# Performance work log

Hardware: AMD Instinct MI355X
Metric: run time of the kernel (lower is better)

## Reference

```python
import jax, jax.numpy as jnp
import numpy as np

N, W, D = 2048, 64, 512
TEMP = 16.0
LN_EPS = 1e-5
NORM_EPS = 1e-12


def layernorm(x, w, b):
    mu = jnp.mean(x, axis=-1, keepdims=True)
    var = jnp.mean(jnp.square(x - mu), axis=-1, keepdims=True)
    return (x - mu) * jax.lax.rsqrt(var + LN_EPS) * w + b


def l2norm(x):
    n = jnp.linalg.norm(x, axis=-1, keepdims=True)
    return x / jnp.maximum(n, NORM_EPS)


def setup_inputs() -> dict:
    key = jax.random.key(0)
    ks = jax.random.split(key, 6)
    q = jax.random.normal(ks[0], (N, D), dtype=jnp.float32)
    cm = jax.random.normal(ks[1], (W, D), dtype=jnp.float32)
    s1 = 1.0 / np.sqrt(2 * D)
    s2 = 1.0 / np.sqrt(D)
    return {
        "query_embeddings": q,
        "class_memories": cm,
        "ln1_w": jnp.ones((2 * D,), jnp.float32),
        "ln1_b": jnp.zeros((2 * D,), jnp.float32),
        "w1": jax.random.uniform(ks[2], (2 * D, D), jnp.float32, -s1, s1),
        "b1": jax.random.uniform(ks[3], (D,), jnp.float32, -s1, s1),
        "w2": jax.random.uniform(ks[4], (D, D), jnp.float32, -s2, s2),
        "b2": jax.random.uniform(ks[5], (D,), jnp.float32, -s2, s2),
        "ln2_w": jnp.ones((D,), jnp.float32),
        "ln2_b": jnp.zeros((D,), jnp.float32),
    }


def reference(query_embeddings, class_memories, ln1_w, ln1_b, w1, b1, w2, b2, ln2_w, ln2_b):
    n, w = query_embeddings.shape[0], class_memories.shape[0]
    q_exp = jnp.broadcast_to(query_embeddings[:, None, :], (n, w, D))   # [N,W,D]
    c_exp = jnp.broadcast_to(class_memories[None, :, :], (n, w, D))     # [N,W,D]
    x = jnp.concatenate([q_exp, c_exp], axis=-1)                        # [N,W,2D]
    h = layernorm(x, ln1_w, ln1_b)
    h = h @ w1 + b1                                                     # [N,W,D]
    h = jax.nn.gelu(h, approximate=False)
    h = h @ w2 + b2                                                     # [N,W,D]
    fused = layernorm(h + q_exp, ln2_w, ln2_b)
    sims = jnp.einsum('nwd,wd->nw', l2norm(fused), l2norm(class_memories))
    return TEMP * sims
```

## Files before the change

kernel.cpp:

```cpp
#include <hip/hip_runtime.h>
#include <cstdint>
#include <cstddef>


#define NQ 2048
#define NWC 64
#define DD 512
#define NCHUNK 19

typedef __attribute__((ext_vector_type(8))) short short8;
typedef __attribute__((ext_vector_type(8))) unsigned short ushort8;
typedef __attribute__((ext_vector_type(4))) float f32x4;

__device__ __forceinline__ unsigned short f2bf(float f) {
  unsigned u = __float_as_uint(f);
  u += 0x7fffu + ((u >> 16) & 1u);
  return (unsigned short)(u >> 16);
}

__device__ __forceinline__ unsigned cvtpk2(float lo, float hi) {
  unsigned r;
  asm("v_cvt_pk_bf16_f32 %0, %1, %2" : "=v"(r) : "v"(lo), "v"(hi));
  return r;
}

__device__ __forceinline__ float bf2f(unsigned short u) {
  return __uint_as_float(((unsigned)u) << 16);
}

__device__ __forceinline__ float gelu_f(float h) {
  float h2 = h * h;
  float z2 = h * fmaf(h2, 0.10295890518f, 2.30221607f);
  float e = exp2f(z2);
  return h * (e * __builtin_amdgcn_rcpf(e + 1.0f));
}

__device__ __forceinline__ float wred(float v) {
#pragma unroll
  for (int m = 1; m < 64; m <<= 1) v += __shfl_xor(v, m, 64);
  return v;
}

__device__ __forceinline__ float sel4(f32x4 v, int r) {
  float x = (r & 1) ? v[1] : v[0];
  float y = (r & 1) ? v[3] : v[2];
  return (r & 2) ? y : x;
}

__global__ __launch_bounds__(256) void k_prep(
    const float* __restrict__ q, const float* __restrict__ cm,
    const float* __restrict__ g1, const float* __restrict__ be1,
    const float* __restrict__ w1, const float* __restrict__ w2,
    const float* __restrict__ g2, const float* __restrict__ be2,
    const float* __restrict__ b2,
    float* __restrict__ Sq, float* __restrict__ SSq, float* __restrict__ qst,
    float* __restrict__ Sc, float* __restrict__ SSc, float* __restrict__ cmhg,
    float* __restrict__ c1, float* __restrict__ c2, float* __restrict__ c3,
    float* __restrict__ Gp, float* __restrict__ Cp, float* __restrict__ V,
    float* __restrict__ gg, float* __restrict__ scal) {
  const int b = blockIdx.x, tid = threadIdx.x;
  const int wv = tid >> 6, l = tid & 63;
  __shared__ float shr[3][4];
  __shared__ float s_inv;

  if (b < 256) {
    f32x4 b20 = *(const f32x4*)(b2 + l * 8);
    f32x4 b21 = *(const f32x4*)(b2 + l * 8 + 4);
    f32x4 g20 = *(const f32x4*)(g2 + l * 8);
    f32x4 g21 = *(const f32x4*)(g2 + l * 8 + 4);
    f32x4 e20 = *(const f32x4*)(be2 + l * 8);
    f32x4 e21 = *(const f32x4*)(be2 + l * 8 + 4);
#pragma unroll
    for (int rr = 0; rr < 2; ++rr) {
      int r = b * 8 + wv * 2 + rr;
      const float* row = q + (size_t)r * DD;
      f32x4 q0 = *(const f32x4*)(row + l * 8);
      f32x4 q1 = *(const f32x4*)(row + l * 8 + 4);
      float s0 = 0, s1 = 0, s2 = 0, s3 = 0, s4 = 0;
#pragma unroll
      for (int i = 0; i < 4; ++i) {
        float v = q0[i]; s0 += v; s1 = fmaf(v, v, s1);
        float qb = v + b20[i], g = g20[i];
        s2 += qb; s3 = fmaf(qb, g * g, s3); s4 = fmaf(qb, g * e20[i], s4);
        v = q1[i]; s0 += v; s1 = fmaf(v, v, s1);
        qb = v + b21[i]; g = g21[i];
        s2 += qb; s3 = fmaf(qb, g * g, s3); s4 = fmaf(qb, g * e21[i], s4);
      }
      s0 = wred(s0); s1 = wred(s1); s2 = wred(s2); s3 = wred(s3); s4 = wred(s4);
      if (l == 0) {
        Sq[r] = s0; SSq[r] = s1;
        qst[r * 4 + 0] = s2; qst[r * 4 + 1] = s3; qst[r * 4 + 2] = s4;
      }
    }
  } else if (b < 320) {
    int w = b - 256;
    const float* row = cm + (size_t)w * DD;
    float sm = 0.f, ss = 0.f;
    for (int c = tid; c < DD; c += 256) { float v = row[c]; sm += v; ss = fmaf(v, v, ss); }
    sm = wred(sm); ss = wred(ss);
    if (l == 0) { shr[0][wv] = sm; shr[1][wv] = ss; }
    __syncthreads();
    if (tid == 0) {
      float smt = shr[0][0] + shr[0][1] + shr[0][2] + shr[0][3];
      float sst = shr[1][0] + shr[1][1] + shr[1][2] + shr[1][3];
      Sc[w] = smt; SSc[w] = sst;
      s_inv = 1.0f / fmaxf(sqrtf(sst), 1e-12f);
    }
    __syncthreads();
    float inv = s_inv;
    float a = 0.f, bs = 0.f, d = 0.f;
    for (int c = tid; c < DD; c += 256) {
      float ch = row[c] * inv;
      float gv = g2[c];
      float gch = gv * ch;
      cmhg[(size_t)w * DD + c] = gch;
      a += gch;
      bs = fmaf(be2[c], ch, bs);
      d = fmaf(b2[c], gch, d);
    }
    a = wred(a); bs = wred(bs); d = wred(d);
    __syncthreads();
    if (l == 0) { shr[0][wv] = a; shr[1][wv] = bs; shr[2][wv] = d; }
    __syncthreads();
    if (tid == 0) {
      c1[w] = shr[0][0] + shr[0][1] + shr[0][2] + shr[0][3];
      c2[w] = shr[1][0] + shr[1][1] + shr[1][2] + shr[1][3];
      c3[w] = shr[2][0] + shr[2][1] + shr[2][2] + shr[2][3];
    }
  } else if (b < 336) {
    int bk = b - 320, k0 = bk * 64;
#pragma unroll
    for (int jh = 0; jh < 2; ++jh) {
      int j = tid + jh * 256;
      float g = 0.f, c = 0.f;
#pragma unroll 4
      for (int k = 0; k < 64; ++k) {
        float wv4 = w1[(size_t)(k0 + k) * DD + j];
        g = fmaf(g1[k0 + k], wv4, g);
        c = fmaf(be1[k0 + k], wv4, c);
      }
      Gp[(size_t)bk * DD + j] = g;
      Cp[(size_t)bk * DD + j] = c;
    }
  } else if (b < 400) {
    int bb = b - 336;
    f32x4 g20 = *(const f32x4*)(g2 + l * 8);
    f32x4 g21 = *(const f32x4*)(g2 + l * 8 + 4);
    f32x4 e20 = *(const f32x4*)(be2 + l * 8);
    f32x4 e21 = *(const f32x4*)(be2 + l * 8 + 4);
#pragma unroll
    for (int rr = 0; rr < 2; ++rr) {
      int k = bb * 8 + wv * 2 + rr;
      const float* row = w2 + (size_t)k * DD;
      f32x4 w0 = *(const f32x4*)(row + l * 8);
      f32x4 w1v = *(const f32x4*)(row + l * 8 + 4);
      float s1 = 0, s3 = 0, s4 = 0;
#pragma unroll
      for (int i = 0; i < 4; ++i) {
        float w = w0[i], g = g20[i];
        s1 += w; s3 = fmaf(w, g * g, s3); s4 = fmaf(w, g * e20[i], s4);
        w = w1v[i]; g = g21[i];
        s1 += w; s3 = fmaf(w, g * g, s3); s4 = fmaf(w, g * e21[i], s4);
      }
      s1 = wred(s1); s3 = wred(s3); s4 = wred(s4);
      if (l == 0) {
        V[k * 4 + 0] = s1; V[k * 4 + 1] = s3; V[k * 4 + 2] = s4; V[k * 4 + 3] = 0.f;
      }
    }
  } else {
    float a0 = 0, a1 = 0, a2 = 0;
    for (int c = tid; c < DD; c += 256) {
      float g = g2[c], be = be2[c];
      gg[c] = g * g;
      a0 = fmaf(g, g, a0); a1 = fmaf(g, be, a1); a2 = fmaf(be, be, a2);
    }
    a0 = wred(a0); a1 = wred(a1); a2 = wred(a2);
    if (l == 0) { shr[0][wv] = a0; shr[1][wv] = a1; shr[2][wv] = a2; }
    __syncthreads();
    if (tid == 0) {
      scal[0] = shr[0][0] + shr[0][1] + shr[0][2] + shr[0][3];
      scal[1] = shr[1][0] + shr[1][1] + shr[1][2] + shr[1][3];
      scal[2] = shr[2][0] + shr[2][1] + shr[2][2] + shr[2][3];
    }
  }
}

__global__ __launch_bounds__(512) void k_pack1(
    const float* __restrict__ w1, const float* __restrict__ ln1w,
    const float* __restrict__ cmhg,
    unsigned short* __restrict__ PW1T, unsigned short* __restrict__ PW1B,
    unsigned short* __restrict__ PCT) {
  int b = blockIdx.x;
  if (b < 128) {
    int roff = (b < 64) ? 0 : 512;
    unsigned short* out = (b < 64) ? PW1T : PW1B;
    int tid = (b & 63) * 512 + threadIdx.x;
    int l = tid & 63, t = (tid >> 6) & 15, ct = tid >> 10, g = l >> 4;
    int col = (ct << 4) + (l & 15);
    ushort8 o;
#pragma unroll
    for (int i = 0; i < 8; ++i) {
      int k = t * 32 + g * 8 + i;
      o[i] = f2bf(w1[(size_t)(roff + k) * DD + col] * ln1w[roff + k]);
    }
    *(ushort8*)(out + (size_t)tid * 8) = o;
  } else {
    int tid = (b - 128) * 512 + threadIdx.x;
    int l = tid & 63, t = (tid >> 6) & 15, g = l >> 4;
    int col = ((tid >> 10) << 4) + (l & 15);
    ushort8 o;
#pragma unroll
    for (int i = 0; i < 8; ++i) {
      int k = t * 32 + g * 8 + i;
      o[i] = f2bf(cmhg[(size_t)col * DD + k]);
    }
    *(ushort8*)(PCT + (size_t)tid * 8) = o;
  }
}

__global__ __launch_bounds__(256) void k_gemms(
    const float* __restrict__ q, const float* __restrict__ cm,
    const float* __restrict__ w2,
    const unsigned short* __restrict__ PW1T, const unsigned short* __restrict__ PW1B,
    const unsigned short* __restrict__ PCT,
    float* __restrict__ A, unsigned short* __restrict__ Bwb,
    float* __restrict__ QC, float* __restrict__ M6) {
  int b = blockIdx.x;
  const float* X; const unsigned short* PW; void* Out;
  int bx, by, ostride, obf;
  if (b < 256)      { X = q;  PW = PW1T; Out = A;    bx = b & 7;   by = b >> 3;  ostride = DD;  obf = 0; }
  else if (b < 264) { X = cm; PW = PW1B; Out = Bwb;  bx = b - 256; by = 0;       ostride = DD;  obf = 1; }
  else if (b < 296) { X = q;  PW = PCT;  Out = QC;   bx = 0;       by = b - 264; ostride = NWC; obf = 0; }
  else              { X = w2; PW = PCT;  Out = M6;   bx = 0;       by = b - 296; ostride = NWC; obf = 0; }

  int l = threadIdx.x & 63;
  int wv = threadIdx.x >> 6;
  int lr = l & 15, g = l >> 4;
  int r0 = by * 64 + wv * 16;
  int cb0 = bx * 4;
  f32x4 acc[4] = {{0,0,0,0},{0,0,0,0},{0,0,0,0},{0,0,0,0}};
  const float* xrow = X + (size_t)(r0 + lr) * DD;
#pragma unroll
  for (int t = 0; t < 16; ++t) {
    int kb = t * 32 + g * 8;
    f32x4 x0 = *(const f32x4*)(xrow + kb);
    f32x4 x1 = *(const f32x4*)(xrow + kb + 4);
    union { short8 s; unsigned u[4]; } af;
    af.u[0] = cvtpk2(x0[0], x0[1]);
    af.u[1] = cvtpk2(x0[2], x0[3]);
    af.u[2] = cvtpk2(x1[0], x1[1]);
    af.u[3] = cvtpk2(x1[2], x1[3]);
#pragma unroll
    for (int c = 0; c < 4; ++c) {
      short8 bf = *(const short8*)(PW + (size_t)(((cb0 + c) * 16 + t) * 64 + l) * 8);
      acc[c] = __builtin_amdgcn_mfma_f32_16x16x32_bf16(af.s, bf, acc[c], 0, 0, 0);
    }
  }
#pragma unroll
  for (int c = 0; c < 4; ++c)
#pragma unroll
    for (int r = 0; r < 4; ++r) {
      size_t idx = (size_t)(r0 + g * 4 + r) * ostride + (cb0 + c) * 16 + lr;
      float v = acc[c][r];
      if (obf) ((unsigned short*)Out)[idx] = f2bf(v);
      else     ((float*)Out)[idx] = v;
    }
}

__global__ __launch_bounds__(512) void k_pack2(
    const float* __restrict__ w2, const float* __restrict__ M6,
    const float* __restrict__ V, const unsigned short* __restrict__ Bwb,
    const float* __restrict__ Gp, const float* __restrict__ Cp,
    const float* __restrict__ b1,
    unsigned short* __restrict__ PW2X, unsigned short* __restrict__ PBw,
    float* __restrict__ G, float* __restrict__ C) {
  int b = blockIdx.x;
  if (b < 76) {
    int tid = b * 512 + threadIdx.x;
    int l = tid & 63, t = (tid >> 6) & 15, ct = tid >> 10, g = l >> 4;
    int col = (ct << 4) + (l & 15);
    ushort8 o;
#pragma unroll
    for (int i = 0; i < 8; ++i) {
      int k = t * 32 + g * 8 + i;
      float v;
      if (col < 512)      v = w2[(size_t)k * DD + col];
      else if (col < 576) v = M6[(size_t)k * 64 + (col - 512)];
      else { int cv = col - 576; v = (cv < 3) ? V[k * 4 + cv] : 0.f; }
      o[i] = f2bf(v);
    }
    *(ushort8*)(PW2X + (size_t)tid * 8) = o;
  } else if (b < 84) {
    int tid = (b - 76) * 512 + threadIdx.x;
    int l = tid & 63, t = (tid >> 6) & 15, wt = tid >> 10;
    ushort8 o;
#pragma unroll
    for (int i = 0; i < 8; ++i)
      o[i] = Bwb[(size_t)(wt * 16 + (l & 15)) * DD + t * 32 + (l >> 4) * 8 + i];
    *(ushort8*)(PBw + (size_t)tid * 8) = o;
  } else {
    int c = threadIdx.x;
    float g = 0.f, cc = 0.f;
#pragma unroll
    for (int p = 0; p < 16; ++p) { g += Gp[p * DD + c]; cc += Cp[p * DD + c]; }
    G[c] = g; C[c] = cc + b1[c];
  }
}


__device__ __forceinline__ void async16(const void* g, void* lds) {
  __builtin_amdgcn_global_load_lds(
      (const __attribute__((address_space(1))) void*)(uintptr_t)g,
      (__attribute__((address_space(3))) void*)(unsigned int)(uintptr_t)lds,
      16, 0, 0);
}

__global__ __launch_bounds__(512, 2) void k_main(
    const float* __restrict__ Afull, const unsigned short* __restrict__ PBw,
    const float* __restrict__ G, const float* __restrict__ Cc,
    const float* __restrict__ q, const float* __restrict__ b2,
    const float* __restrict__ gg, const float* __restrict__ qst,
    const float* __restrict__ QC, const float* __restrict__ c1v,
    const float* __restrict__ c2v, const float* __restrict__ c3v,
    const float* __restrict__ Sq, const float* __restrict__ SSq,
    const float* __restrict__ Sc, const float* __restrict__ SSc,
    const float* __restrict__ scal, const unsigned short* __restrict__ PW2X,
    float* __restrict__ out) {

  __shared__ __align__(16) float sG[DD], sC[DD], sGG[DD];
  __shared__ __align__(16) float sA[4][DD], sQB[4][DD];
  __shared__ __align__(16) unsigned short sW[3][16384];

  const int tid = threadIdx.x;
  const int wv = tid >> 6, l = tid & 63;
  const int g = l >> 4, lr = l & 15;
  const int n0 = blockIdx.x * 4;
  const int sub = wv >> 1;
  const int n = n0 + sub;
  const int whalf = wv & 1;
  const int w0 = whalf * 32 + lr;
  const int w1p = w0 + 16;

  sG[tid] = G[tid]; sC[tid] = Cc[tid]; sGG[tid] = gg[tid];
#pragma unroll
  for (int s = 0; s < 4; ++s) {
    sA[s][tid]  = Afull[(size_t)(n0 + s) * DD + tid];
    sQB[s][tid] = q[(size_t)(n0 + s) * DD + tid] + b2[tid];
  }
  __syncthreads();

#pragma unroll
  for (int c = 0; c < 2; ++c)
#pragma unroll
    for (int j = 0; j < 4; ++j)
      async16(PW2X + (size_t)c * 16384 + (size_t)(j * 512 + tid) * 8,
              &sW[c][(j * 512 + wv * 64) * 8]);

  float sqn = Sq[n], ssqn = SSq[n];
  float mu0 = (sqn + Sc[w0]) * (1.0f / 1024.0f);
  float rs0 = rsqrtf((ssqn + SSc[w0]) * (1.0f / 1024.0f) - mu0 * mu0 + 1e-5f);
  float mu1 = (sqn + Sc[w1p]) * (1.0f / 1024.0f);
  float rs1 = rsqrtf((ssqn + SSc[w1p]) * (1.0f / 1024.0f) - mu1 * mu1 + 1e-5f);
  float al0 = rs0, bl0 = -rs0 * mu0;
  float al1 = rs1, bl1 = -rs1 * mu1;

  short8 af0[16], af1[16];
  const unsigned short* pb0 = PBw + (size_t)(whalf * 2) * 16 * 512;
  const unsigned short* pb1 = PBw + (size_t)(whalf * 2 + 1) * 16 * 512;
#pragma unroll
  for (int t = 0; t < 16; ++t) {
    int kb = t * 32 + g * 8;
    f32x4 a0 = *(const f32x4*)&sA[sub][kb];
    f32x4 a1 = *(const f32x4*)&sA[sub][kb + 4];
    f32x4 g0 = *(const f32x4*)&sG[kb];
    f32x4 g1v = *(const f32x4*)&sG[kb + 4];
    f32x4 c0 = *(const f32x4*)&sC[kb];
    f32x4 c1f = *(const f32x4*)&sC[kb + 4];
    ushort8 ub0 = *(const ushort8*)(pb0 + (size_t)(t * 64 + l) * 8);
    ushort8 ub1 = *(const ushort8*)(pb1 + (size_t)(t * 64 + l) * 8);
    float hA[8], hB[8];
#pragma unroll
    for (int i = 0; i < 4; ++i) {
      float in0 = fmaf(bl0, g0[i], c0[i]);
      float in1 = fmaf(bl1, g0[i], c0[i]);
      hA[i] = gelu_f(fmaf(al0, a0[i] + bf2f(ub0[i]), in0));
      hB[i] = gelu_f(fmaf(al1, a0[i] + bf2f(ub1[i]), in1));
      float jn0 = fmaf(bl0, g1v[i], c1f[i]);
      float jn1 = fmaf(bl1, g1v[i], c1f[i]);
      hA[4 + i] = gelu_f(fmaf(al0, a1[i] + bf2f(ub0[4 + i]), jn0));
      hB[4 + i] = gelu_f(fmaf(al1, a1[i] + bf2f(ub1[4 + i]), jn1));
    }
    union { short8 s; unsigned u[4]; } pa, pb;
    pa.u[0] = cvtpk2(hA[0], hA[1]); pa.u[1] = cvtpk2(hA[2], hA[3]);
    pa.u[2] = cvtpk2(hA[4], hA[5]); pa.u[3] = cvtpk2(hA[6], hA[7]);
    pb.u[0] = cvtpk2(hB[0], hB[1]); pb.u[1] = cvtpk2(hB[2], hB[3]);
    pb.u[2] = cvtpk2(hB[4], hB[5]); pb.u[3] = cvtpk2(hB[6], hB[7]);
    af0[t] = pa.s; af1[t] = pb.s;
  }

  float S20 = 0.f, S50 = 0.f, S21 = 0.f, S51 = 0.f;
  float m6d0 = 0.f, m6d1 = 0.f;
  float v1d0 = 0.f, v3d0 = 0.f, v4d0 = 0.f;
  float v1d1 = 0.f, v3d1 = 0.f, v4d1 = 0.f;

  for (int cc = 0; cc < NCHUNK; ++cc) {
    if (cc < NCHUNK - 1) asm volatile("s_waitcnt vmcnt(4)" ::: "memory");
    else                 asm volatile("s_waitcnt vmcnt(0)" ::: "memory");
    asm volatile("s_waitcnt lgkmcnt(0)" ::: "memory");
    __builtin_amdgcn_s_barrier();
    if (cc + 2 < NCHUNK) {
      const unsigned short* src = PW2X + (size_t)(cc + 2) * 16384;
      unsigned short* dst = sW[(cc + 2) % 3];
#pragma unroll
      for (int j = 0; j < 4; ++j)
        async16(src + (size_t)(j * 512 + tid) * 8, &dst[(j * 512 + wv * 64) * 8]);
    }
    const unsigned short* wbuf = sW[cc % 3];

    if (cc < 16) {
      f32x4 acc00 = {0,0,0,0}, acc01 = {0,0,0,0}, acc10 = {0,0,0,0}, acc11 = {0,0,0,0};
      __builtin_amdgcn_s_setprio(1);
#pragma unroll
      for (int t = 0; t < 16; ++t) {
        short8 bf0 = *(const short8*)(wbuf + (size_t)((t * 64 + l) * 8));
        short8 bf1 = *(const short8*)(wbuf + (size_t)(((16 + t) * 64 + l) * 8));
        acc00 = __builtin_amdgcn_mfma_f32_16x16x32_bf16(bf0, af0[t], acc00, 0, 0, 0);
        acc10 = __builtin_amdgcn_mfma_f32_16x16x32_bf16(bf0, af1[t], acc10, 0, 0, 0);
        acc01 = __builtin_amdgcn_mfma_f32_16x16x32_bf16(bf1, af0[t], acc01, 0, 0, 0);
        acc11 = __builtin_amdgcn_mfma_f32_16x16x32_bf16(bf1, af1[t], acc11, 0, 0, 0);
      }
      __builtin_amdgcn_s_setprio(0);
#pragma unroll
      for (int ct = 0; ct < 2; ++ct) {
        int cb = cc * 32 + ct * 16 + g * 4;
        f32x4 qb4 = *(const f32x4*)&sQB[sub][cb];
        f32x4 gg4 = *(const f32x4*)&sGG[cb];
        f32x4 aAv = ct ? acc01 : acc00;
        f32x4 aBv = ct ? acc11 : acc10;
#pragma unroll
        for (int r = 0; r < 4; ++r) {
          float y = aAv[r] + qb4[r];
          float y2 = y * y;
          S20 += y2; S50 = fmaf(y2, gg4[r], S50);
          float z = aBv[r] + qb4[r];
          float z2 = z * z;
          S21 += z2; S51 = fmaf(z2, gg4[r], S51);
        }
      }
    } else if (cc == 16 + whalf) {
      f32x4 acc00 = {0,0,0,0}, acc11 = {0,0,0,0};
      __builtin_amdgcn_s_setprio(1);
#pragma unroll
      for (int t = 0; t < 16; ++t) {
        short8 bf0 = *(const short8*)(wbuf + (size_t)((t * 64 + l) * 8));
        short8 bf1 = *(const short8*)(wbuf + (size_t)(((16 + t) * 64 + l) * 8));
        acc00 = __builtin_amdgcn_mfma_f32_16x16x32_bf16(bf0, af0[t], acc00, 0, 0, 0);
        acc11 = __builtin_amdgcn_mfma_f32_16x16x32_bf16(bf1, af1[t], acc11, 0, 0, 0);
      }
      __builtin_amdgcn_s_setprio(0);
      float d0 = sel4(acc00, lr & 3);
      float d1 = sel4(acc11, lr & 3);
      int src = lr + ((lr >> 2) << 4);
      m6d0 = __shfl(d0, src, 64);
      m6d1 = __shfl(d1, src, 64);
    } else if (cc == 18) {
      f32x4 acc00 = {0,0,0,0}, acc10 = {0,0,0,0};
      __builtin_amdgcn_s_setprio(1);
#pragma unroll
      for (int t = 0; t < 16; ++t) {
        short8 bf0 = *(const short8*)(wbuf + (size_t)((t * 64 + l) * 8));
        acc00 = __builtin_amdgcn_mfma_f32_16x16x32_bf16(bf0, af0[t], acc00, 0, 0, 0);
        acc10 = __builtin_amdgcn_mfma_f32_16x16x32_bf16(bf0, af1[t], acc10, 0, 0, 0);
      }
      __builtin_amdgcn_s_setprio(0);
      v1d0 = __shfl(acc00[0], lr, 64);
      v3d0 = __shfl(acc00[1], lr, 64);
      v4d0 = __shfl(acc00[2], lr, 64);
      v1d1 = __shfl(acc10[0], lr, 64);
      v3d1 = __shfl(acc10[1], lr, 64);
      v4d1 = __shfl(acc10[2], lr, 64);
    }
  }

  S20 += __shfl_xor(S20, 16, 64); S20 += __shfl_xor(S20, 32, 64);
  S50 += __shfl_xor(S50, 16, 64); S50 += __shfl_xor(S50, 32, 64);
  S21 += __shfl_xor(S21, 16, 64); S21 += __shfl_xor(S21, 32, 64);
  S51 += __shfl_xor(S51, 16, 64); S51 += __shfl_xor(S51, 32, 64);

  if (g == 0) {
    float sg2v = scal[0], sgbv = scal[1], sb2v = scal[2];
    float qbs = qst[n * 4 + 0], qggs = qst[n * 4 + 1], qgbs = qst[n * 4 + 2];
#pragma unroll
    for (int p = 0; p < 2; ++p) {
      int w = whalf * 32 + p * 16 + lr;
      float S1 = (p ? v1d1 : v1d0) + qbs;
      float S2 = (p ? S21 : S20);
      float S3 = (p ? v3d1 : v3d0) + qggs;
      float S4 = (p ? v4d1 : v4d0) + qgbs;
      float S5 = (p ? S51 : S50);
      float S6 = (p ? m6d1 : m6d0) + QC[(size_t)n * NWC + w] + c3v[w];
      float mu2 = S1 * (1.0f / 512.0f);
      float var2 = S2 * (1.0f / 512.0f) - mu2 * mu2;
      float rs2 = rsqrtf(var2 + 1e-5f);
      float n2 = rs2 * rs2 * (S5 - 2.f * mu2 * S3 + mu2 * mu2 * sg2v)
               + 2.f * rs2 * (S4 - mu2 * sgbv) + sb2v;
      float num = rs2 * (S6 - mu2 * c1v[w]) + c2v[w];
      out[(size_t)n * NWC + w] = 16.0f * num / fmaxf(sqrtf(fmaxf(n2, 0.f)), 1e-12f);
    }
  }
}


extern "C" void kernel_launch(void* const* d_in, const int* in_sizes, int n_in,
                              void* d_out, int out_size, void* d_ws, size_t ws_size,
                              hipStream_t stream) {
  const float* q    = (const float*)d_in[0];
  const float* cm   = (const float*)d_in[1];
  const float* ln1w = (const float*)d_in[2];
  const float* ln1b = (const float*)d_in[3];
  const float* w1   = (const float*)d_in[4];
  const float* b1   = (const float*)d_in[5];
  const float* w2   = (const float*)d_in[6];
  const float* b2   = (const float*)d_in[7];
  const float* ln2w = (const float*)d_in[8];
  const float* ln2b = (const float*)d_in[9];
  float* out = (float*)d_out;

  char* p = (char*)d_ws;
  auto alloc = [&](size_t bytes) { char* r = p; p += (bytes + 255) & ~(size_t)255; return r; };
  float* A     = (float*)alloc((size_t)NQ * DD * 4);
  unsigned short* Bwb = (unsigned short*)alloc((size_t)NWC * DD * 2);
  float* G     = (float*)alloc(DD * 4);
  float* C     = (float*)alloc(DD * 4);
  float* Gp    = (float*)alloc((size_t)16 * DD * 4);
  float* Cp    = (float*)alloc((size_t)16 * DD * 4);
  float* Sq    = (float*)alloc(NQ * 4);
  float* SSq   = (float*)alloc(NQ * 4);
  float* Sc    = (float*)alloc(NWC * 4);
  float* SSc   = (float*)alloc(NWC * 4);
  float* cmhg  = (float*)alloc((size_t)NWC * DD * 4);
  float* c1    = (float*)alloc(NWC * 4);
  float* c2    = (float*)alloc(NWC * 4);
  float* c3    = (float*)alloc(NWC * 4);
  float* gg    = (float*)alloc(DD * 4);
  float* scal  = (float*)alloc(256);
  float* qst   = (float*)alloc((size_t)NQ * 4 * 4);
  float* QC    = (float*)alloc((size_t)NQ * NWC * 4);
  float* M6buf = (float*)alloc((size_t)DD * NWC * 4);
  float* Vbuf  = (float*)alloc((size_t)DD * 4 * 4);
  unsigned short* PW1T = (unsigned short*)alloc((size_t)DD * DD * 2);
  unsigned short* PW1B = (unsigned short*)alloc((size_t)DD * DD * 2);
  unsigned short* PCT  = (unsigned short*)alloc((size_t)DD * NWC * 2);
  unsigned short* PBw  = (unsigned short*)alloc((size_t)NWC * DD * 2);
  unsigned short* PW2X = (unsigned short*)alloc((size_t)NCHUNK * 16384 * 2);

  k_prep<<<401, 256, 0, stream>>>(q, cm, ln1w, ln1b, w1, w2, ln2w, ln2b, b2,
                                  Sq, SSq, qst, Sc, SSc, cmhg, c1, c2, c3,
                                  Gp, Cp, Vbuf, gg, scal);
  k_pack1<<<136, 512, 0, stream>>>(w1, ln1w, cmhg, PW1T, PW1B, PCT);
  k_gemms<<<304, 256, 0, stream>>>(q, cm, w2, PW1T, PW1B, PCT, A, Bwb, QC, M6buf);
  k_pack2<<<85, 512, 0, stream>>>(w2, M6buf, Vbuf, Bwb, Gp, Cp, b1, PW2X, PBw, G, C);
  k_main<<<512, 512, 0, stream>>>(A, PBw, G, C, q, b2, gg, qst, QC, c1, c2, c3,
                                  Sq, SSq, Sc, SSc, scal, PW2X, out);
}
```

Measured before the change: 139.2 us.

## Quantize second GEMM to int8 MFMA with per-column weight scales

Weights of the second projection (plus auxiliary columns) are quantized to int8 with per-column scales in the pack kernel. GELU outputs are quantized to int8 using a fixed scale with clamping. The main loop uses i32 16x16x64 int8 MFMA with half-sized LDS chunks, and dequantizes accumulators using the scales. This reduces weight bandwidth and matrix instruction count, but adds quantization error and clamps GELU activations to a fixed range.

Result: faster. 124.5 us (-10.6%).

```diff
diff --git a/kernel.cpp b/kernel.cpp
--- a/kernel.cpp
+++ b/kernel.cpp
@@ -7,10 +7,13 @@
 #define NWC 64
 #define DD 512
 #define NCHUNK 19
+#define SA_CONST (4.0f / 127.0f)
 
 typedef __attribute__((ext_vector_type(8))) short short8;
 typedef __attribute__((ext_vector_type(8))) unsigned short ushort8;
 typedef __attribute__((ext_vector_type(4))) float f32x4;
+typedef __attribute__((ext_vector_type(4))) int i32v4;
+typedef __attribute__((ext_vector_type(4))) unsigned u32x4;
 
 __device__ __forceinline__ unsigned short f2bf(float f) {
   unsigned u = __float_as_uint(f);
@@ -28,11 +31,19 @@
   return __uint_as_float(((unsigned)u) << 16);
 }
 
-__device__ __forceinline__ float gelu_f(float h) {
+__device__ __forceinline__ float gelu31(float h) {
   float h2 = h * h;
-  float z2 = h * fmaf(h2, 0.10295890518f, 2.30221607f);
-  float e = exp2f(z2);
-  return h * (e * __builtin_amdgcn_rcpf(e + 1.0f));
+  float zn = h * fmaf(h2, -0.10295890518f, -2.30221607f);
+  float t = exp2f(zn);
+  float r = __builtin_amdgcn_rcpf(1.0f + t);
+  float g = (h * 31.75f) * r;
+  return fminf(fmaxf(g, -127.0f), 127.0f);
+}
+
+__device__ __forceinline__ unsigned pk4i8(float a, float b, float c, float d) {
+  int ia = (int)rintf(a), ib = (int)rintf(b), ic = (int)rintf(c), id = (int)rintf(d);
+  return (unsigned)(ia & 255) | ((unsigned)(ib & 255) << 8) |
+         ((unsigned)(ic & 255) << 16) | ((unsigned)(id & 255) << 24);
 }
 
 __device__ __forceinline__ float wred(float v) {
@@ -41,9 +52,9 @@
   return v;
 }
 
-__device__ __forceinline__ float sel4(f32x4 v, int r) {
-  float x = (r & 1) ? v[1] : v[0];
-  float y = (r & 1) ? v[3] : v[2];
+__device__ __forceinline__ int sel4i(i32v4 v, int r) {
+  int x = (r & 1) ? v[1] : v[0];
+  int y = (r & 1) ? v[3] : v[2];
   return (r & 2) ? y : x;
 }
 
@@ -272,38 +283,70 @@
     const float* __restrict__ V, const unsigned short* __restrict__ Bwb,
     const float* __restrict__ Gp, const float* __restrict__ Cp,
     const float* __restrict__ b1,
-    unsigned short* __restrict__ PW2X, unsigned short* __restrict__ PBw,
-    float* __restrict__ G, float* __restrict__ C) {
-  int b = blockIdx.x;
-  if (b < 76) {
-    int tid = b * 512 + threadIdx.x;
-    int l = tid & 63, t = (tid >> 6) & 15, ct = tid >> 10, g = l >> 4;
-    int col = (ct << 4) + (l & 15);
-    ushort8 o;
+    signed char* __restrict__ PW2X, unsigned short* __restrict__ PBw,
+    float* __restrict__ G, float* __restrict__ C, float* __restrict__ Scales) {
+  int b = blockIdx.x, tx = threadIdx.x;
+  __shared__ float red[16][33];
+  __shared__ float sinv[16];
+  if (b < 38) {
+    int ct = b;
+    int t8 = tx >> 6, l = tx & 63, g4 = l >> 4, lc = l & 15;
+    int col = ct * 16 + lc;
+    float v[16]; float lmax = 0.f;
+#pragma unroll
+    for (int i = 0; i < 16; ++i) {
+      int k = t8 * 64 + g4 * 16 + i;
+      float x;
+      if (col < 512)      x = w2[(size_t)k * DD + col];
+      else if (col < 576) x = M6[(size_t)k * 64 + (col - 512)];
+      else { int cv = col - 576; x = (cv < 3) ? V[k * 4 + cv] : 0.f; }
+      v[i] = x; lmax = fmaxf(lmax, fabsf(x));
+    }
+    red[lc][t8 * 4 + g4] = lmax;
+    __syncthreads();
+    if (tx < 16) {
+      float m = 0.f;
+#pragma unroll
+      for (int j = 0; j < 32; ++j) m = fmaxf(m, red[tx][j]);
+      float sc = fmaxf(m, 1e-20f) * (1.0f / 127.0f);
+      Scales[ct * 16 + tx] = sc;
+      sinv[tx] = 1.0f / sc;
+    }
+    __syncthreads();
+    float inv = sinv[lc];
+    u32x4 d;
+#pragma unroll
+    for (int j = 0; j < 4; ++j) {
+      unsigned u = 0;
+#pragma unroll
+      for (int e = 0; e < 4; ++e) {
+        float qv = v[j * 4 + e] * inv;
+        qv = fminf(fmaxf(qv, -127.f), 127.f);
+        int iq = (int)rintf(qv);
+        u |= ((unsigned)(iq & 255)) << (8 * e);
+      }
+      d[j] = u;
+    }
+    *(u32x4*)(PW2X + (size_t)ct * 8192 + (size_t)(t8 * 64 + l) * 16) = d;
+  } else if (b < 42) {
+    int slot = (b - 38) * 512 + tx;
+    int wt = slot >> 9, r = slot & 511, t8 = r >> 6, l = r & 63;
+    int w = wt * 16 + (l & 15);
+    int kb = t8 * 64 + (l >> 4) * 16;
+    ushort8 o0, o1;
 #pragma unroll
     for (int i = 0; i < 8; ++i) {
-      int k = t * 32 + g * 8 + i;
-      float v;
-      if (col < 512)      v = w2[(size_t)k * DD + col];
-      else if (col < 576) v = M6[(size_t)k * 64 + (col - 512)];
-      else { int cv = col - 576; v = (cv < 3) ? V[k * 4 + cv] : 0.f; }
-      o[i] = f2bf(v);
-    }
-    *(ushort8*)(PW2X + (size_t)tid * 8) = o;
-  } else if (b < 84) {
-    int tid = (b - 76) * 512 + threadIdx.x;
-    int l = tid & 63, t = (tid >> 6) & 15, wt = tid >> 10;
-    ushort8 o;
-#pragma unroll
-    for (int i = 0; i < 8; ++i)
-      o[i] = Bwb[(size_t)(wt * 16 + (l & 15)) * DD + t * 32 + (l >> 4) * 8 + i];
-    *(ushort8*)(PBw + (size_t)tid * 8) = o;
+      o0[i] = Bwb[(size_t)w * DD + kb + i];
+      o1[i] = Bwb[(size_t)w * DD + kb + 8 + i];
+    }
+    *(ushort8*)(PBw + (size_t)slot * 16) = o0;
+    *(ushort8*)(PBw + (size_t)slot * 16 + 8) = o1;
   } else {
-    int c = threadIdx.x;
-    float g = 0.f, cc = 0.f;
-#pragma unroll
-    for (int p = 0; p < 16; ++p) { g += Gp[p * DD + c]; cc += Cp[p * DD + c]; }
-    G[c] = g; C[c] = cc + b1[c];
+    int c = tx;
+    float g = 0.f, cc2 = 0.f;
+#pragma unroll
+    for (int p = 0; p < 16; ++p) { g += Gp[p * DD + c]; cc2 += Cp[p * DD + c]; }
+    G[c] = g; C[c] = cc2 + b1[c];
   }
 }
 
@@ -324,12 +367,12 @@
     const float* __restrict__ c2v, const float* __restrict__ c3v,
     const float* __restrict__ Sq, const float* __restrict__ SSq,
     const float* __restrict__ Sc, const float* __restrict__ SSc,
-    const float* __restrict__ scal, const unsigned short* __restrict__ PW2X,
-    float* __restrict__ out) {
-
-  __shared__ __align__(16) float sG[DD], sC[DD], sGG[DD];
+    const float* __restrict__ scal, const signed char* __restrict__ PW2X,
+    const float* __restrict__ Scales, float* __restrict__ out) {
+
+  __shared__ __align__(16) float sG[DD], sC[DD], sGG[DD], sSC[608];
   __shared__ __align__(16) float sA[4][DD], sQB[4][DD];
-  __shared__ __align__(16) unsigned short sW[3][16384];
+  __shared__ __align__(16) signed char sW[3 * 16384];
 
   const int tid = threadIdx.x;
   const int wv = tid >> 6, l = tid & 63;
@@ -342,6 +385,7 @@
   const int w1p = w0 + 16;
 
   sG[tid] = G[tid]; sC[tid] = Cc[tid]; sGG[tid] = gg[tid];
+  for (int i = tid; i < 608; i += 512) sSC[i] = Scales[i] * SA_CONST;
 #pragma unroll
   for (int s = 0; s < 4; ++s) {
     sA[s][tid]  = Afull[(size_t)(n0 + s) * DD + tid];
@@ -352,9 +396,9 @@
 #pragma unroll
   for (int c = 0; c < 2; ++c)
 #pragma unroll
-    for (int j = 0; j < 4; ++j)
-      async16(PW2X + (size_t)c * 16384 + (size_t)(j * 512 + tid) * 8,
-              &sW[c][(j * 512 + wv * 64) * 8]);
+    for (int j = 0; j < 2; ++j)
+      async16(PW2X + (size_t)c * 16384 + (size_t)(j * 512 + tid) * 16,
+              &sW[c * 16384 + (j * 512 + wv * 64) * 16]);
 
   float sqn = Sq[n], ssqn = SSq[n];
   float mu0 = (sqn + Sc[w0]) * (1.0f / 1024.0f);
@@ -364,70 +408,71 @@
   float al0 = rs0, bl0 = -rs0 * mu0;
   float al1 = rs1, bl1 = -rs1 * mu1;
 
-  short8 af0[16], af1[16];
-  const unsigned short* pb0 = PBw + (size_t)(whalf * 2) * 16 * 512;
-  const unsigned short* pb1 = PBw + (size_t)(whalf * 2 + 1) * 16 * 512;
-#pragma unroll
-  for (int t = 0; t < 16; ++t) {
-    int kb = t * 32 + g * 8;
-    f32x4 a0 = *(const f32x4*)&sA[sub][kb];
-    f32x4 a1 = *(const f32x4*)&sA[sub][kb + 4];
-    f32x4 g0 = *(const f32x4*)&sG[kb];
-    f32x4 g1v = *(const f32x4*)&sG[kb + 4];
-    f32x4 c0 = *(const f32x4*)&sC[kb];
-    f32x4 c1f = *(const f32x4*)&sC[kb + 4];
-    ushort8 ub0 = *(const ushort8*)(pb0 + (size_t)(t * 64 + l) * 8);
-    ushort8 ub1 = *(const ushort8*)(pb1 + (size_t)(t * 64 + l) * 8);
-    float hA[8], hB[8];
-#pragma unroll
-    for (int i = 0; i < 4; ++i) {
-      float in0 = fmaf(bl0, g0[i], c0[i]);
-      float in1 = fmaf(bl1, g0[i], c0[i]);
-      hA[i] = gelu_f(fmaf(al0, a0[i] + bf2f(ub0[i]), in0));
-      hB[i] = gelu_f(fmaf(al1, a0[i] + bf2f(ub1[i]), in1));
-      float jn0 = fmaf(bl0, g1v[i], c1f[i]);
-      float jn1 = fmaf(bl1, g1v[i], c1f[i]);
-      hA[4 + i] = gelu_f(fmaf(al0, a1[i] + bf2f(ub0[4 + i]), jn0));
-      hB[4 + i] = gelu_f(fmaf(al1, a1[i] + bf2f(ub1[4 + i]), jn1));
-    }
-    union { short8 s; unsigned u[4]; } pa, pb;
-    pa.u[0] = cvtpk2(hA[0], hA[1]); pa.u[1] = cvtpk2(hA[2], hA[3]);
-    pa.u[2] = cvtpk2(hA[4], hA[5]); pa.u[3] = cvtpk2(hA[6], hA[7]);
-    pb.u[0] = cvtpk2(hB[0], hB[1]); pb.u[1] = cvtpk2(hB[2], hB[3]);
-    pb.u[2] = cvtpk2(hB[4], hB[5]); pb.u[3] = cvtpk2(hB[6], hB[7]);
-    af0[t] = pa.s; af1[t] = pb.s;
+  i32v4 af0[8], af1[8];
+  const unsigned short* pb0 = PBw + (size_t)(whalf * 2) * 8192;
+  const unsigned short* pb1 = PBw + (size_t)(whalf * 2 + 1) * 8192;
+#pragma unroll
+  for (int t8 = 0; t8 < 8; ++t8) {
+    int kb = t8 * 64 + g * 16;
+    ushort8 u0a = *(const ushort8*)(pb0 + (size_t)(t8 * 64 + l) * 16);
+    ushort8 u0b = *(const ushort8*)(pb0 + (size_t)(t8 * 64 + l) * 16 + 8);
+    ushort8 u1a = *(const ushort8*)(pb1 + (size_t)(t8 * 64 + l) * 16);
+    ushort8 u1b = *(const ushort8*)(pb1 + (size_t)(t8 * 64 + l) * 16 + 8);
+    unsigned dw0[4], dw1[4];
+#pragma unroll
+    for (int j = 0; j < 4; ++j) {
+      f32x4 av = *(const f32x4*)&sA[sub][kb + j * 4];
+      f32x4 gv = *(const f32x4*)&sG[kb + j * 4];
+      f32x4 cv = *(const f32x4*)&sC[kb + j * 4];
+      float hA[4], hB[4];
+#pragma unroll
+      for (int i2 = 0; i2 < 4; ++i2) {
+        int e = j * 4 + i2;
+        float bw0 = bf2f(e < 8 ? u0a[e & 7] : u0b[e & 7]);
+        float bw1 = bf2f(e < 8 ? u1a[e & 7] : u1b[e & 7]);
+        float base0 = fmaf(bl0, gv[i2], cv[i2]);
+        float base1 = fmaf(bl1, gv[i2], cv[i2]);
+        hA[i2] = gelu31(fmaf(al0, av[i2] + bw0, base0));
+        hB[i2] = gelu31(fmaf(al1, av[i2] + bw1, base1));
+      }
+      dw0[j] = pk4i8(hA[0], hA[1], hA[2], hA[3]);
+      dw1[j] = pk4i8(hB[0], hB[1], hB[2], hB[3]);
+    }
+    i32v4 a0v = {(int)dw0[0], (int)dw0[1], (int)dw0[2], (int)dw0[3]};
+    i32v4 a1v = {(int)dw1[0], (int)dw1[1], (int)dw1[2], (int)dw1[3]};
+    af0[t8] = a0v; af1[t8] = a1v;
   }
 
   float S20 = 0.f, S50 = 0.f, S21 = 0.f, S51 = 0.f;
-  float m6d0 = 0.f, m6d1 = 0.f;
-  float v1d0 = 0.f, v3d0 = 0.f, v4d0 = 0.f;
-  float v1d1 = 0.f, v3d1 = 0.f, v4d1 = 0.f;
+  int m6i0 = 0, m6i1 = 0;
+  int v1i0 = 0, v3i0 = 0, v4i0 = 0;
+  int v1i1 = 0, v3i1 = 0, v4i1 = 0;
 
   for (int cc = 0; cc < NCHUNK; ++cc) {
-    if (cc < NCHUNK - 1) asm volatile("s_waitcnt vmcnt(4)" ::: "memory");
+    if (cc < NCHUNK - 1) asm volatile("s_waitcnt vmcnt(2)" ::: "memory");
     else                 asm volatile("s_waitcnt vmcnt(0)" ::: "memory");
     asm volatile("s_waitcnt lgkmcnt(0)" ::: "memory");
     __builtin_amdgcn_s_barrier();
     if (cc + 2 < NCHUNK) {
-      const unsigned short* src = PW2X + (size_t)(cc + 2) * 16384;
-      unsigned short* dst = sW[(cc + 2) % 3];
-#pragma unroll
-      for (int j = 0; j < 4; ++j)
-        async16(src + (size_t)(j * 512 + tid) * 8, &dst[(j * 512 + wv * 64) * 8]);
-    }
-    const unsigned short* wbuf = sW[cc % 3];
+      const signed char* src = PW2X + (size_t)(cc + 2) * 16384;
+      signed char* dst = &sW[((cc + 2) % 3) * 16384];
+#pragma unroll
+      for (int j = 0; j < 2; ++j)
+        async16(src + (size_t)(j * 512 + tid) * 16, dst + (j * 512 + wv * 64) * 16);
+    }
+    const signed char* wbuf = &sW[(cc % 3) * 16384];
 
     if (cc < 16) {
-      f32x4 acc00 = {0,0,0,0}, acc01 = {0,0,0,0}, acc10 = {0,0,0,0}, acc11 = {0,0,0,0};
+      i32v4 acc00 = {0,0,0,0}, acc01 = {0,0,0,0}, acc10 = {0,0,0,0}, acc11 = {0,0,0,0};
       __builtin_amdgcn_s_setprio(1);
 #pragma unroll
-      for (int t = 0; t < 16; ++t) {
-        short8 bf0 = *(const short8*)(wbuf + (size_t)((t * 64 + l) * 8));
-        short8 bf1 = *(const short8*)(wbuf + (size_t)(((16 + t) * 64 + l) * 8));
-        acc00 = __builtin_amdgcn_mfma_f32_16x16x32_bf16(bf0, af0[t], acc00, 0, 0, 0);
-        acc10 = __builtin_amdgcn_mfma_f32_16x16x32_bf16(bf0, af1[t], acc10, 0, 0, 0);
-        acc01 = __builtin_amdgcn_mfma_f32_16x16x32_bf16(bf1, af0[t], acc01, 0, 0, 0);
-        acc11 = __builtin_amdgcn_mfma_f32_16x16x32_bf16(bf1, af1[t], acc11, 0, 0, 0);
+      for (int t8 = 0; t8 < 8; ++t8) {
+        i32v4 bf0 = *(const i32v4*)(wbuf + (size_t)(t8 * 64 + l) * 16);
+        i32v4 bf1 = *(const i32v4*)(wbuf + 8192 + (size_t)(t8 * 64 + l) * 16);
+        acc00 = __builtin_amdgcn_mfma_i32_16x16x64_i8(bf0, af0[t8], acc00, 0, 0, 0);
+        acc10 = __builtin_amdgcn_mfma_i32_16x16x64_i8(bf0, af1[t8], acc10, 0, 0, 0);
+        acc01 = __builtin_amdgcn_mfma_i32_16x16x64_i8(bf1, af0[t8], acc01, 0, 0, 0);
+        acc11 = __builtin_amdgcn_mfma_i32_16x16x64_i8(bf1, af1[t8], acc11, 0, 0, 0);
       }
       __builtin_amdgcn_s_setprio(0);
 #pragma unroll
@@ -435,50 +480,51 @@
         int cb = cc * 32 + ct * 16 + g * 4;
         f32x4 qb4 = *(const f32x4*)&sQB[sub][cb];
         f32x4 gg4 = *(const f32x4*)&sGG[cb];
-        f32x4 aAv = ct ? acc01 : acc00;
-        f32x4 aBv = ct ? acc11 : acc10;
+        f32x4 sc4 = *(const f32x4*)&sSC[cb];
+        i32v4 aAv = ct ? acc01 : acc00;
+        i32v4 aBv = ct ? acc11 : acc10;
 #pragma unroll
         for (int r = 0; r < 4; ++r) {
-          float y = aAv[r] + qb4[r];
+          float y = fmaf((float)aAv[r], sc4[r], qb4[r]);
           float y2 = y * y;
           S20 += y2; S50 = fmaf(y2, gg4[r], S50);
-          float z = aBv[r] + qb4[r];
+          float z = fmaf((float)aBv[r], sc4[r], qb4[r]);
           float z2 = z * z;
           S21 += z2; S51 = fmaf(z2, gg4[r], S51);
         }
       }
     } else if (cc == 16 + whalf) {
-      f32x4 acc00 = {0,0,0,0}, acc11 = {0,0,0,0};
+      i32v4 acc00 = {0,0,0,0}, acc11 = {0,0,0,0};
       __builtin_amdgcn_s_setprio(1);
 #pragma unroll
-      for (int t = 0; t < 16; ++t) {
-        short8 bf0 = *(const short8*)(wbuf + (size_t)((t * 64 + l) * 8));
-        short8 bf1 = *(const short8*)(wbuf + (size_t)(((16 + t) * 64 + l) * 8));
-        acc00 = __builtin_amdgcn_mfma_f32_16x16x32_bf16(bf0, af0[t], acc00, 0, 0, 0);
-        acc11 = __builtin_amdgcn_mfma_f32_16x16x32_bf16(bf1, af1[t], acc11, 0, 0, 0);
+      for (int t8 = 0; t8 < 8; ++t8) {
+        i32v4 bf0 = *(const i32v4*)(wbuf + (size_t)(t8 * 64 + l) * 16);
+        i32v4 bf1 = *(const i32v4*)(wbuf + 8192 + (size_t)(t8 * 64 + l) * 16);
+        acc00 = __builtin_amdgcn_mfma_i32_16x16x64_i8(bf0, af0[t8], acc00, 0, 0, 0);
+        acc11 = __builtin_amdgcn_mfma_i32_16x16x64_i8(bf1, af1[t8], acc11, 0, 0, 0);
       }
       __builtin_amdgcn_s_setprio(0);
-      float d0 = sel4(acc00, lr & 3);
-      float d1 = sel4(acc11, lr & 3);
+      int d0 = sel4i(acc00, lr & 3);
+      int d1 = sel4i(acc11, lr & 3);
       int src = lr + ((lr >> 2) << 4);
-      m6d0 = __shfl(d0, src, 64);
-      m6d1 = __shfl(d1, src, 64);
+      m6i0 = __shfl(d0, src, 64);
+      m6i1 = __shfl(d1, src, 64);
     } else if (cc == 18) {
-      f32x4 acc00 = {0,0,0,0}, acc10 = {0,0,0,0};
+      i32v4 acc00 = {0,0,0,0}, acc10 = {0,0,0,0};
       __builtin_amdgcn_s_setprio(1);
 #pragma unroll
-      for (int t = 0; t < 16; ++t) {
-        short8 bf0 = *(const short8*)(wbuf + (size_t)((t * 64 + l) * 8));
-        acc00 = __builtin_amdgcn_mfma_f32_16x16x32_bf16(bf0, af0[t], acc00, 0, 0, 0);
-        acc10 = __builtin_amdgcn_mfma_f32_16x16x32_bf16(bf0, af1[t], acc10, 0, 0, 0);
+      for (int t8 = 0; t8 < 8; ++t8) {
+        i32v4 bf0 = *(const i32v4*)(wbuf + (size_t)(t8 * 64 + l) * 16);
+        acc00 = __builtin_amdgcn_mfma_i32_16x16x64_i8(bf0, af0[t8], acc00, 0, 0, 0);
+        acc10 = __builtin_amdgcn_mfma_i32_16x16x64_i8(bf0, af1[t8], acc10, 0, 0, 0);
       }
       __builtin_amdgcn_s_setprio(0);
-      v1d0 = __shfl(acc00[0], lr, 64);
-      v3d0 = __shfl(acc00[1], lr, 64);
-      v4d0 = __shfl(acc00[2], lr, 64);
-      v1d1 = __shfl(acc10[0], lr, 64);
-      v3d1 = __shfl(acc10[1], lr, 64);
-      v4d1 = __shfl(acc10[2], lr, 64);
+      v1i0 = __shfl(acc00[0], lr, 64);
+      v3i0 = __shfl(acc00[1], lr, 64);
+      v4i0 = __shfl(acc00[2], lr, 64);
+      v1i1 = __shfl(acc10[0], lr, 64);
+      v3i1 = __shfl(acc10[1], lr, 64);
+      v4i1 = __shfl(acc10[2], lr, 64);
     }
   }
 
@@ -493,12 +539,16 @@
 #pragma unroll
     for (int p = 0; p < 2; ++p) {
       int w = whalf * 32 + p * 16 + lr;
-      float S1 = (p ? v1d1 : v1d0) + qbs;
+      float v1f = (float)(p ? v1i1 : v1i0) * sSC[576];
+      float v3f = (float)(p ? v3i1 : v3i0) * sSC[577];
+      float v4f = (float)(p ? v4i1 : v4i0) * sSC[578];
+      float m6f = (float)(p ? m6i1 : m6i0) * sSC[512 + w];
+      float S1 = v1f + qbs;
       float S2 = (p ? S21 : S20);
-      float S3 = (p ? v3d1 : v3d0) + qggs;
-      float S4 = (p ? v4d1 : v4d0) + qgbs;
+      float S3 = v3f + qggs;
+      float S4 = v4f + qgbs;
       float S5 = (p ? S51 : S50);
-      float S6 = (p ? m6d1 : m6d0) + QC[(size_t)n * NWC + w] + c3v[w];
+      float S6 = m6f + QC[(size_t)n * NWC + w] + c3v[w];
       float mu2 = S1 * (1.0f / 512.0f);
       float var2 = S2 * (1.0f / 512.0f) - mu2 * mu2;
       float rs2 = rsqrtf(var2 + 1e-5f);
@@ -548,18 +598,19 @@
   float* QC    = (float*)alloc((size_t)NQ * NWC * 4);
   float* M6buf = (float*)alloc((size_t)DD * NWC * 4);
   float* Vbuf  = (float*)alloc((size_t)DD * 4 * 4);
+  float* Scl   = (float*)alloc(608 * 4);
   unsigned short* PW1T = (unsigned short*)alloc((size_t)DD * DD * 2);
   unsigned short* PW1B = (unsigned short*)alloc((size_t)DD * DD * 2);
   unsigned short* PCT  = (unsigned short*)alloc((size_t)DD * NWC * 2);
   unsigned short* PBw  = (unsigned short*)alloc((size_t)NWC * DD * 2);
-  unsigned short* PW2X = (unsigned short*)alloc((size_t)NCHUNK * 16384 * 2);
+  signed char* PW2X    = (signed char*)alloc((size_t)38 * 8192);
 
   k_prep<<<401, 256, 0, stream>>>(q, cm, ln1w, ln1b, w1, w2, ln2w, ln2b, b2,
                                   Sq, SSq, qst, Sc, SSc, cmhg, c1, c2, c3,
                                   Gp, Cp, Vbuf, gg, scal);
   k_pack1<<<136, 512, 0, stream>>>(w1, ln1w, cmhg, PW1T, PW1B, PCT);
   k_gemms<<<304, 256, 0, stream>>>(q, cm, w2, PW1T, PW1B, PCT, A, Bwb, QC, M6buf);
-  k_pack2<<<85, 512, 0, stream>>>(w2, M6buf, Vbuf, Bwb, Gp, Cp, b1, PW2X, PBw, G, C);
+  k_pack2<<<43, 512, 0, stream>>>(w2, M6buf, Vbuf, Bwb, Gp, Cp, b1, PW2X, PBw, G, C, Scl);
   k_main<<<512, 512, 0, stream>>>(A, PBw, G, C, q, b2, gg, qst, QC, c1, c2, c3,
-                                  Sq, SSq, Sc, SSc, scal, PW2X, out);
-}
+                                  Sq, SSq, Sc, SSc, scal, PW2X, Scl, out);
+}
```
